# Performance work log

Hardware: AMD Instinct MI355X
Metric: run time of the kernel (lower is better)

The kernel has to match this reference:

```python
import jax, jax.numpy as jnp
import numpy as np
import math

N_LEVELS = 16
F_PER_LEVEL = 2
LOG2_T = 19
T = 1 << LOG2_T
BASE_RES = 16
MAX_RES = 2048
PER_LEVEL_SCALE = (MAX_RES / BASE_RES) ** (1.0 / (N_LEVELS - 1))
BOUND = 0.5
PRIMES = (np.uint32(1), np.uint32(2654435761), np.uint32(805459861))


def _weight_norm(v, g):
    # w = g * v / ||v||_row (torch weight_norm over dim=1)
    return v * (g / jnp.linalg.norm(v, axis=1))[:, None]


def _softplus100(x):
    # torch Softplus(beta=100)
    return jax.nn.softplus(100.0 * x) * 0.01


def hashgrid_encode(x01, table):
    # x01: [N,3] in [0,1]; table: [L, T, F]
    feats = []
    for l in range(N_LEVELS):
        scale = BASE_RES * (PER_LEVEL_SCALE ** l) - 1.0  # tcnn grid scale
        res = int(math.ceil(scale)) + 1
        pos = x01 * scale + 0.5
        pos_floor = jnp.floor(pos)
        w = pos - pos_floor                      # [N,3] trilinear fracs
        c0 = pos_floor.astype(jnp.uint32)        # [N,3] base corner
        dense = (res ** 3) <= T                  # static per level
        acc = jnp.zeros((x01.shape[0], F_PER_LEVEL), dtype=table.dtype)
        for corner in range(8):
            off = [(corner >> d) & 1 for d in range(3)]
            cx = c0[:, 0] + np.uint32(off[0])
            cy = c0[:, 1] + np.uint32(off[1])
            cz = c0[:, 2] + np.uint32(off[2])
            if dense:
                idx = cx + cy * np.uint32(res) + cz * np.uint32(res * res)
            else:
                idx = (cx * PRIMES[0]) ^ (cy * PRIMES[1]) ^ (cz * PRIMES[2])
                idx = idx & np.uint32(T - 1)
            wc = ((w[:, 0] if off[0] else 1.0 - w[:, 0])
                  * (w[:, 1] if off[1] else 1.0 - w[:, 1])
                  * (w[:, 2] if off[2] else 1.0 - w[:, 2]))
            acc = acc + wc[:, None] * table[l, idx.astype(jnp.int32)]
        feats.append(acc)
    return jnp.concatenate(feats, axis=-1)  # [N, 32]


def setup_inputs() -> dict:
    key = jax.random.key(0)
    ks = jax.random.split(key, 4)
    N = 2 ** 21
    x = jax.random.uniform(ks[0], (N, 3), jnp.float32, -BOUND, BOUND)
    table = jax.random.uniform(ks[1], (N_LEVELS, T, F_PER_LEVEL), jnp.float32, -1e-4, 1e-4)
    d_in, d_hid, d_out = 35, 64, 13
    v1 = jax.random.normal(ks[2], (d_hid, d_in), jnp.float32) * (math.sqrt(2) / math.sqrt(d_hid))
    v2 = jax.random.normal(ks[3], (d_out, d_hid), jnp.float32) * 1e-4 + math.sqrt(math.pi) / math.sqrt(d_hid)
    g1 = jnp.linalg.norm(v1, axis=1)
    g2 = jnp.linalg.norm(v2, axis=1)
    b1 = jnp.zeros((d_hid,), jnp.float32)
    b2 = jnp.full((d_out,), -0.5, jnp.float32)  # -sphere_init_radius
    return {"x": x, "table": table, "v1": v1, "g1": g1, "b1": b1,
            "v2": v2, "g2": g2, "b2": b2}


def reference(x, table, v1, g1, b1, v2, g2, b2):
    x01 = jnp.clip((x + BOUND) / (2.0 * BOUND), 0.0, 1.0)
    enc = hashgrid_encode(x01, table)            # [N, 32]
    h = jnp.concatenate([x, enc], axis=1)        # [N, 35]
    w1 = _weight_norm(v1, g1)
    w2 = _weight_norm(v2, g2)
    h = _softplus100(h @ w1.T + b1)
    out = h @ w2.T + b2                          # [N, 13]
    return out
```

## Files before the change

kernel.cpp:

```cpp
#include <hip/hip_runtime.h>
#include <hip/hip_fp16.h>
#include <cstdint>
#include <cmath>

#define NLEV 16
#define NHASH 11
#define NDENSE 5
#define TBL (1u << 19)
#define NBKT 32768

typedef _Float16 half8 __attribute__((ext_vector_type(8)));
typedef float f32x4 __attribute__((ext_vector_type(4)));
typedef float f32x4v __attribute__((ext_vector_type(4)));

struct LevelParams {
    float scale[NLEV];
    uint32_t res[NLEV];
    uint32_t hashed_mask;
};

__device__ __forceinline__ int krow_map(int kr) {
    if (kr <= 2) return kr;
    if (kr >= 4 && kr <= 13) return kr - 1;
    if (kr >= 16 && kr <= 37) return kr - 3;
    return -1;
}

__global__ __launch_bounds__(256) void prep_weights(
    const float* __restrict__ v1, const float* __restrict__ g1,
    const float* __restrict__ v2, const float* __restrict__ g2,
    float* __restrict__ w1t, float* __restrict__ w2n,
    __half* __restrict__ w1f, __half* __restrict__ w2f)
{
    int t = threadIdx.x;
    if (t < 64) {
        float s = 0.f;
        #pragma unroll
        for (int k = 0; k < 35; ++k) { float v = v1[t*35 + k]; s += v*v; }
        float f = g1[t] / sqrtf(s);
        #pragma unroll
        for (int k = 0; k < 35; ++k) w1t[k*64 + t] = v1[t*35 + k] * f;
    } else if (t < 77) {
        int r = t - 64;
        float s = 0.f;
        #pragma unroll
        for (int k = 0; k < 64; ++k) { float v = v2[r*64 + k]; s += v*v; }
        float f = g2[r] / sqrtf(s);
        #pragma unroll
        for (int k = 0; k < 64; ++k) w2n[r*64 + k] = v2[r*64 + k] * f;
    }
    __syncthreads();
    for (int i = t; i < 4096; i += 256) {
        int j = i & 7, lane = (i >> 3) & 63, nt = (i >> 9) & 3, kc = i >> 11;
        int kr = kc*32 + ((lane >> 4) << 3) + j;
        int ncol = nt*16 + (lane & 15);
        int m = krow_map(kr);
        float val = (m >= 0) ? w1t[m*64 + ncol] : 0.f;
        w1f[i] = __float2half(val);
    }
    for (int i = t; i < 1024; i += 256) {
        int j = i & 7, lane = (i >> 3) & 63, kc = i >> 9;
        int kr = kc*32 + ((lane >> 4) << 3) + j;
        int col = lane & 15;
        float val = (col < 13) ? w2n[col*64 + kr] : 0.f;
        w2f[i] = __float2half(val);
    }
}

__global__ __launch_bounds__(256) void pack_table(
    const float2* __restrict__ in, uint32_t* __restrict__ out, int n)
{
    int i = blockIdx.x * 256 + threadIdx.x;
    if (i < n) {
        float2 v = in[i];
        __half2 h = __floats2half2_rn(v.x, v.y);
        out[i] = *reinterpret_cast<uint32_t*>(&h);
    }
}

__device__ __forceinline__ uint32_t bucket_key(float u0, float u1, float u2)
{
    uint32_t a = min(31u, (uint32_t)(u0 * 32.f));
    uint32_t b = min(31u, (uint32_t)(u1 * 32.f));
    uint32_t c = min(31u, (uint32_t)(u2 * 32.f));
    return (a << 10) | (b << 5) | c;
}

__device__ __forceinline__ void load_u(const float* __restrict__ x, int pp,
                                       float& u0, float& u1, float& u2)
{
    float x0 = x[3*(size_t)pp + 0];
    float x1 = x[3*(size_t)pp + 1];
    float x2 = x[3*(size_t)pp + 2];
    u0 = fminf(fmaxf(x0 + 0.5f, 0.f), 1.f);
    u1 = fminf(fmaxf(x1 + 0.5f, 0.f), 1.f);
    u2 = fminf(fmaxf(x2 + 0.5f, 0.f), 1.f);
}

__global__ __launch_bounds__(256) void hist_kernel(
    const float* __restrict__ x, uint32_t* __restrict__ hist, int N)
{
    int i = blockIdx.x * 256 + threadIdx.x;
    if (i < N) {
        float u0, u1, u2;
        load_u(x, i, u0, u1, u2);
        atomicAdd(&hist[bucket_key(u0, u1, u2)], 1u);
    }
}

__global__ __launch_bounds__(1024) void scan_hist(
    const uint32_t* __restrict__ hist, uint32_t* __restrict__ offs)
{
    __shared__ uint32_t part[1024];
    int t = threadIdx.x;
    uint32_t loc[32];
    uint32_t s = 0;
    #pragma unroll
    for (int k = 0; k < 32; ++k) { loc[k] = s; s += hist[t*32 + k]; }
    part[t] = s;
    __syncthreads();
    for (int d = 1; d < 1024; d <<= 1) {
        uint32_t v = (t >= d) ? part[t - d] : 0u;
        __syncthreads();
        part[t] += v;
        __syncthreads();
    }
    uint32_t base = (t > 0) ? part[t - 1] : 0u;
    #pragma unroll
    for (int k = 0; k < 32; ++k) offs[t*32 + k] = base + loc[k];
}

__global__ __launch_bounds__(256) void scatter_kernel(
    const float* __restrict__ x, uint32_t* __restrict__ offs,
    float4* __restrict__ xs4, int N)
{
    int i = blockIdx.x * 256 + threadIdx.x;
    if (i < N) {
        float x0 = x[3*(size_t)i + 0];
        float x1 = x[3*(size_t)i + 1];
        float x2 = x[3*(size_t)i + 2];
        float u0 = fminf(fmaxf(x0 + 0.5f, 0.f), 1.f);
        float u1 = fminf(fmaxf(x1 + 0.5f, 0.f), 1.f);
        float u2 = fminf(fmaxf(x2 + 0.5f, 0.f), 1.f);
        uint32_t pos = atomicAdd(&offs[bucket_key(u0, u1, u2)], 1u);
        xs4[pos] = make_float4(x0, x1, x2, __int_as_float(i));
    }
}

__device__ __forceinline__ void encode_one(
    float u0, float u1, float u2, float s, uint32_t res, bool hashed,
    const uint32_t* __restrict__ tl, float& a0, float& a1)
{
    float px = u0 * s + 0.5f;
    float py = u1 * s + 0.5f;
    float pz = u2 * s + 0.5f;
    float fx = floorf(px), fy = floorf(py), fz = floorf(pz);
    float wx1 = px - fx, wy1 = py - fy, wz1 = pz - fz;
    float wx0 = 1.f - wx1, wy0 = 1.f - wy1, wz0 = 1.f - wz1;
    uint32_t cx = (uint32_t)fx, cy = (uint32_t)fy, cz = (uint32_t)fz;

    uint32_t ix0, ix1, iy0, iy1, iz0, iz1;
    if (hashed) {
        ix0 = cx;                 ix1 = cx + 1u;
        iy0 = cy * 2654435761u;   iy1 = (cy + 1u) * 2654435761u;
        iz0 = cz * 805459861u;    iz1 = (cz + 1u) * 805459861u;
    } else {
        ix0 = cx;                 ix1 = cx + 1u;
        iy0 = cy * res;           iy1 = iy0 + res;
        uint32_t rr = res * res;
        iz0 = cz * rr;            iz1 = iz0 + rr;
    }

    uint32_t idxs[8];
    #pragma unroll
    for (int c = 0; c < 8; ++c) {
        uint32_t jx = (c & 1) ? ix1 : ix0;
        uint32_t jy = (c & 2) ? iy1 : iy0;
        uint32_t jz = (c & 4) ? iz1 : iz0;
        idxs[c] = hashed ? ((jx ^ jy ^ jz) & (TBL - 1u)) : (jx + jy + jz);
    }
    uint32_t raw[8];
    #pragma unroll
    for (int c = 0; c < 8; ++c) raw[c] = tl[idxs[c]];

    float wxy00 = wx0*wy0, wxy10 = wx1*wy0, wxy01 = wx0*wy1, wxy11 = wx1*wy1;
    a0 = 0.f; a1 = 0.f;
    #pragma unroll
    for (int c = 0; c < 8; ++c) {
        float wxy = (c & 2) ? ((c & 1) ? wxy11 : wxy01)
                            : ((c & 1) ? wxy10 : wxy00);
        float w = wxy * ((c & 4) ? wz1 : wz0);
        __half2 hv = *reinterpret_cast<__half2*>(&raw[c]);
        float2 v = __half22float2(hv);
        a0 += w * v.x;
        a1 += w * v.y;
    }
}

template <int SORTED>
__global__ __launch_bounds__(256) void encode_hashed(
    const float* __restrict__ x, const float4* __restrict__ xs4,
    const uint32_t* __restrict__ tpk,
    uint32_t* __restrict__ feats, int N, int chunks_per_level, int lbase,
    LevelParams P)
{
    int bid = blockIdx.x;
    int ll = bid / chunks_per_level;
    int l = lbase + ll;
    int li = l - NDENSE;
    int base = (bid - ll * chunks_per_level) * 512 + threadIdx.x;
    const uint32_t* tl = tpk + (size_t)l * TBL;
    float s = P.scale[l];

    int p[2] = { base, base + 256 };
    uint2 Q[2][4];
    uint32_t par[2];
    float wx0[2], wx1[2], wyz[2][4];

    #pragma unroll
    for (int t = 0; t < 2; ++t) {
        int pp = (p[t] < N) ? p[t] : (N - 1);
        float u0, u1, u2;
        if (SORTED) {
            f32x4v v4 = __builtin_nontemporal_load(
                reinterpret_cast<const f32x4v*>(xs4 + pp));
            u0 = fminf(fmaxf(v4.x + 0.5f, 0.f), 1.f);
            u1 = fminf(fmaxf(v4.y + 0.5f, 0.f), 1.f);
            u2 = fminf(fmaxf(v4.z + 0.5f, 0.f), 1.f);
        } else {
            load_u(x, pp, u0, u1, u2);
        }

        float px = u0 * s + 0.5f;
        float py = u1 * s + 0.5f;
        float pz = u2 * s + 0.5f;
        float fx = floorf(px), fy = floorf(py), fz = floorf(pz);
        float a1f = px - fx, b1f = py - fy, c1f = pz - fz;
        wx1[t] = a1f; wx0[t] = 1.f - a1f;
        float wy0 = 1.f - b1f, wz0 = 1.f - c1f;
        uint32_t cx = (uint32_t)fx, cy = (uint32_t)fy, cz = (uint32_t)fz;

        wyz[t][0] = wy0 * wz0;
        wyz[t][1] = b1f * wz0;
        wyz[t][2] = wy0 * c1f;
        wyz[t][3] = b1f * c1f;

        uint32_t hy0 = cy * 2654435761u, hy1 = (cy + 1u) * 2654435761u;
        uint32_t hz0 = cz * 805459861u,  hz1 = (cz + 1u) * 805459861u;
        uint32_t r[4] = { hy0 ^ hz0, hy1 ^ hz0, hy0 ^ hz1, hy1 ^ hz1 };

        par[t] = 0u;
        if (!(cx & 1u)) {
            #pragma unroll
            for (int k = 0; k < 4; ++k) {
                uint32_t v0 = (cx ^ r[k]) & (TBL - 1u);
                Q[t][k] = *reinterpret_cast<const uint2*>(tl + (v0 & ~1u));
                par[t] |= (v0 & 1u) << k;
            }
        } else {
            #pragma unroll
            for (int k = 0; k < 4; ++k) {
                uint32_t v0 = (cx ^ r[k]) & (TBL - 1u);
                uint32_t v1 = ((cx + 1u) ^ r[k]) & (TBL - 1u);
                Q[t][k].x = tl[v0];
                Q[t][k].y = tl[v1];
            }
        }
    }

    #pragma unroll
    for (int t = 0; t < 2; ++t) {
        float a0 = 0.f, a1 = 0.f;
        #pragma unroll
        for (int k = 0; k < 4; ++k) {
            uint32_t swap = (par[t] >> k) & 1u;
            uint32_t b0 = swap ? Q[t][k].y : Q[t][k].x;
            uint32_t b1 = swap ? Q[t][k].x : Q[t][k].y;
            __half2 h0 = *reinterpret_cast<__half2*>(&b0);
            __half2 h1 = *reinterpret_cast<__half2*>(&b1);
            float2 c0 = __half22float2(h0);
            float2 c1 = __half22float2(h1);
            a0 += wyz[t][k] * (wx0[t] * c0.x + wx1[t] * c1.x);
            a1 += wyz[t][k] * (wx0[t] * c0.y + wx1[t] * c1.y);
        }
        __half2 hv = __floats2half2_rn(a0, a1);
        if (p[t] < N) {
            __builtin_nontemporal_store(*reinterpret_cast<uint32_t*>(&hv),
                                        &feats[(size_t)li * N + p[t]]);
        }
    }
}

__global__ __launch_bounds__(256) void mlp_mfma(
    const float4* __restrict__ xs4,
    const uint32_t* __restrict__ tpk,
    const uint32_t* __restrict__ feats,
    const __half* __restrict__ w1f,
    const __half* __restrict__ w2f,
    const float* __restrict__ b1,
    const float* __restrict__ b2,
    float* __restrict__ out, int N, LevelParams P)
{
    __shared__ uint4 ldsA[4][576];
    __shared__ int   ldsI[4][64];
    int wid = threadIdx.x >> 6, lane = threadIdx.x & 63;
    int wpt = blockIdx.x * 256 + wid * 64;
    int pt = wpt + lane;
    int pp = (pt < N) ? pt : (N - 1);

    f32x4v v4 = __builtin_nontemporal_load(
        reinterpret_cast<const f32x4v*>(xs4 + pp));
    float x0 = v4.x, x1 = v4.y, x2 = v4.z;
    ldsI[wid][lane] = __float_as_int(v4.w);
    float u0 = fminf(fmaxf(x0 + 0.5f, 0.f), 1.f);
    float u1 = fminf(fmaxf(x1 + 0.5f, 0.f), 1.f);
    float u2 = fminf(fmaxf(x2 + 0.5f, 0.f), 1.f);

    uint32_t dw[32];
    #pragma unroll
    for (int i = 0; i < 32; ++i) dw[i] = 0u;
    __half2 h01 = __floats2half2_rn(x0, x1);
    __half2 h2_ = __floats2half2_rn(x2, 0.f);
    dw[0] = *reinterpret_cast<uint32_t*>(&h01);
    dw[1] = *reinterpret_cast<uint32_t*>(&h2_);
    #pragma unroll
    for (int l = 0; l < NDENSE; ++l) {
        const uint32_t* tl = tpk + (size_t)l * TBL;
        float a0, a1;
        encode_one(u0, u1, u2, P.scale[l], P.res[l], false, tl, a0, a1);
        __half2 hv = __floats2half2_rn(a0, a1);
        dw[2 + l] = *reinterpret_cast<uint32_t*>(&hv);
    }
    #pragma unroll
    for (int li = 0; li < NHASH; ++li)
        dw[8 + li] = __builtin_nontemporal_load(&feats[(size_t)li * N + pp]);

    #pragma unroll
    for (int c = 0; c < 8; ++c) {
        uint4 ch = make_uint4(dw[4*c], dw[4*c+1], dw[4*c+2], dw[4*c+3]);
        ldsA[wid][c*64 + lane] = ch;
    }

    const uint4* w1f4 = (const uint4*)w1f;
    half8 bf[4][2];
    #pragma unroll
    for (int nt = 0; nt < 4; ++nt)
        #pragma unroll
        for (int kc = 0; kc < 2; ++kc) {
            uint4 u = w1f4[(kc*4 + nt)*64 + lane];
            bf[nt][kc] = __builtin_bit_cast(half8, u);
        }

    f32x4 C[4][4];
    #pragma unroll
    for (int nt = 0; nt < 4; ++nt) {
        float bv = b1[nt*16 + (lane & 15)];
        #pragma unroll
        for (int m = 0; m < 4; ++m) C[m][nt] = f32x4{bv, bv, bv, bv};
    }

    #pragma unroll
    for (int m = 0; m < 4; ++m) {
        uint4 ua0 = ldsA[wid][((lane >> 4)      )*64 + m*16 + (lane & 15)];
        uint4 ua1 = ldsA[wid][((lane >> 4) + 4  )*64 + m*16 + (lane & 15)];
        half8 a0 = __builtin_bit_cast(half8, ua0);
        half8 a1 = __builtin_bit_cast(half8, ua1);
        #pragma unroll
        for (int nt = 0; nt < 4; ++nt) {
            C[m][nt] = __builtin_amdgcn_mfma_f32_16x16x32_f16(a0, bf[nt][0], C[m][nt], 0, 0, 0);
            C[m][nt] = __builtin_amdgcn_mfma_f32_16x16x32_f16(a1, bf[nt][1], C[m][nt], 0, 0, 0);
        }
    }

    #pragma unroll
    for (int m = 0; m < 4; ++m)
        #pragma unroll
        for (int nt = 0; nt < 4; ++nt)
            #pragma unroll
            for (int r = 0; r < 4; ++r) {
                float z = 100.f * C[m][nt][r];
                float t = __expf(-fabsf(z));
                C[m][nt][r] = (fmaxf(z, 0.f) + __logf(1.f + t)) * 0.01f;
            }

    uint32_t* hl = (uint32_t*)&ldsA[wid][0];
    bool evenl = (lane & 1) == 0;
    #pragma unroll
    for (int m = 0; m < 4; ++m)
        #pragma unroll
        for (int nt = 0; nt < 4; ++nt)
            #pragma unroll
            for (int r = 0; r < 4; ++r) {
                float self = C[m][nt][r];
                float other = __shfl_xor(self, 1);
                if (evenl) {
                    __half2 hp = __floats2half2_rn(self, other);
                    int prow = m*16 + ((lane >> 4) << 2) + r;
                    int colp = (nt*16 + (lane & 15)) >> 1;
                    hl[prow*36 + colp] = *reinterpret_cast<uint32_t*>(&hp);
                }
            }

    const uint4* w2f4 = (const uint4*)w2f;
    half8 b2f[2];
    #pragma unroll
    for (int kc = 0; kc < 2; ++kc) {
        uint4 u = w2f4[kc*64 + lane];
        b2f[kc] = __builtin_bit_cast(half8, u);
    }
    int col = lane & 15;
    float b2v = (col < 13) ? b2[col] : 0.f;

    #pragma unroll
    for (int m = 0; m < 4; ++m) {
        uint4 ua0 = ldsA[wid][(m*16 + col)*9 + 0 + (lane >> 4)];
        uint4 ua1 = ldsA[wid][(m*16 + col)*9 + 4 + (lane >> 4)];
        f32x4 c2 = f32x4{b2v, b2v, b2v, b2v};
        c2 = __builtin_amdgcn_mfma_f32_16x16x32_f16(
                 __builtin_bit_cast(half8, ua0), b2f[0], c2, 0, 0, 0);
        c2 = __builtin_amdgcn_mfma_f32_16x16x32_f16(
                 __builtin_bit_cast(half8, ua1), b2f[1], c2, 0, 0, 0);
        #pragma unroll
        for (int r = 0; r < 4; ++r) {
            int prow = m*16 + ((lane >> 4) << 2) + r;
            if (col < 13 && wpt + prow < N) {
                int og = ldsI[wid][prow];
                out[(size_t)og * 13 + col] = c2[r];
            }
        }
    }
}

__global__ __launch_bounds__(256) void mlp_dense_scalar(
    const float* __restrict__ x, const uint32_t* __restrict__ tpk,
    const uint32_t* __restrict__ feats,
    const float* __restrict__ w1t, const float* __restrict__ b1,
    const float* __restrict__ w2, const float* __restrict__ b2,
    float* __restrict__ out, int N, LevelParams P)
{
    int p = blockIdx.x * 256 + threadIdx.x;
    bool valid = (p < N);
    int pp = valid ? p : (N - 1);

    float x0 = x[3*(size_t)pp + 0];
    float x1 = x[3*(size_t)pp + 1];
    float x2 = x[3*(size_t)pp + 2];
    float u0 = fminf(fmaxf(x0 + 0.5f, 0.f), 1.f);
    float u1 = fminf(fmaxf(x1 + 0.5f, 0.f), 1.f);
    float u2 = fminf(fmaxf(x2 + 0.5f, 0.f), 1.f);

    uint32_t rf[NHASH];
    #pragma unroll
    for (int li = 0; li < NHASH; ++li) rf[li] = feats[(size_t)li * N + pp];

    float h[64];
    #pragma unroll
    for (int j = 0; j < 64; ++j)
        h[j] = b1[j] + x0 * w1t[0*64 + j] + x1 * w1t[1*64 + j] + x2 * w1t[2*64 + j];

    #pragma unroll
    for (int l = 0; l < NDENSE; ++l) {
        const uint32_t* tl = tpk + (size_t)l * TBL;
        float a0, a1;
        encode_one(u0, u1, u2, P.scale[l], P.res[l], false, tl, a0, a1);
        const float* c0p = w1t + (3 + 2*l) * 64;
        const float* c1p = c0p + 64;
        #pragma unroll
        for (int j = 0; j < 64; ++j) h[j] += a0 * c0p[j] + a1 * c1p[j];
    }
    #pragma unroll
    for (int li = 0; li < NHASH; ++li) {
        __half2 hv = *reinterpret_cast<__half2*>(&rf[li]);
        float2 f = __half22float2(hv);
        int l = li + NDENSE;
        const float* c0p = w1t + (3 + 2*l) * 64;
        const float* c1p = c0p + 64;
        #pragma unroll
        for (int j = 0; j < 64; ++j) h[j] += f.x * c0p[j] + f.y * c1p[j];
    }
    #pragma unroll
    for (int j = 0; j < 64; ++j) {
        float z = 100.f * h[j];
        float t = __expf(-fabsf(z));
        h[j] = (fmaxf(z, 0.f) + __logf(1.f + t)) * 0.01f;
    }
    float* op = out + (size_t)pp * 13;
    for (int o = 0; o < 13; ++o) {
        float a = b2[o];
        const float* wr = w2 + o * 64;
        #pragma unroll
        for (int k = 0; k < 64; ++k) a = fmaf(h[k], wr[k], a);
        if (valid) op[o] = a;
    }
}

template <int PACKED>
__global__ __launch_bounds__(256) void sdf_fused(
    const float* __restrict__ x, const void* __restrict__ table,
    const float* __restrict__ w1t, const float* __restrict__ b1,
    const float* __restrict__ w2, const float* __restrict__ b2,
    float* __restrict__ out, int N, LevelParams P)
{
    int i = blockIdx.x * 256 + threadIdx.x;
    bool valid = (i < N);
    int ii = valid ? i : (N - 1);

    float x0 = x[3*(size_t)ii + 0];
    float x1 = x[3*(size_t)ii + 1];
    float x2 = x[3*(size_t)ii + 2];
    float u0 = fminf(fmaxf(x0 + 0.5f, 0.f), 1.f);
    float u1 = fminf(fmaxf(x1 + 0.5f, 0.f), 1.f);
    float u2 = fminf(fmaxf(x2 + 0.5f, 0.f), 1.f);

    float h[64];
    #pragma unroll
    for (int j = 0; j < 64; ++j)
        h[j] = b1[j] + x0 * w1t[0*64 + j] + x1 * w1t[1*64 + j] + x2 * w1t[2*64 + j];

    for (int l = 0; l < NLEV; ++l) {
        bool hashed = (P.hashed_mask >> l) & 1u;
        float a0, a1;
        if (PACKED) {
            const uint32_t* tl = (const uint32_t*)table + (size_t)l * TBL;
            encode_one(u0, u1, u2, P.scale[l], P.res[l], hashed, tl, a0, a1);
        } else {
            const float* tl = (const float*)table + (size_t)l * (size_t)(TBL * 2u);
            float s = P.scale[l]; uint32_t res = P.res[l];
            float px = u0*s + 0.5f, py = u1*s + 0.5f, pz = u2*s + 0.5f;
            float fx = floorf(px), fy = floorf(py), fz = floorf(pz);
            float wx1 = px-fx, wy1 = py-fy, wz1 = pz-fz;
            float wx0 = 1.f-wx1, wy0 = 1.f-wy1, wz0 = 1.f-wz1;
            uint32_t cx = (uint32_t)fx, cy = (uint32_t)fy, cz = (uint32_t)fz;
            a0 = 0.f; a1 = 0.f;
            #pragma unroll
            for (int c = 0; c < 8; ++c) {
                uint32_t jx = cx + (c & 1);
                uint32_t jy = cy + ((c >> 1) & 1);
                uint32_t jz = cz + ((c >> 2) & 1);
                uint32_t idx = hashed
                    ? ((jx ^ (jy * 2654435761u) ^ (jz * 805459861u)) & (TBL - 1u))
                    : (jx + jy * res + jz * res * res);
                float w = ((c & 1) ? wx1 : wx0) * ((c & 2) ? wy1 : wy0)
                        * ((c & 4) ? wz1 : wz0);
                float2 v = *reinterpret_cast<const float2*>(tl + (size_t)idx * 2u);
                a0 += w * v.x; a1 += w * v.y;
            }
        }
        const float* c0p = w1t + (3 + 2*l) * 64;
        const float* c1p = c0p + 64;
        #pragma unroll
        for (int j = 0; j < 64; ++j) h[j] += a0 * c0p[j] + a1 * c1p[j];
    }

    #pragma unroll
    for (int j = 0; j < 64; ++j) {
        float z = 100.f * h[j];
        float t = __expf(-fabsf(z));
        h[j] = (fmaxf(z, 0.f) + __logf(1.f + t)) * 0.01f;
    }

    float* op = out + (size_t)ii * 13;
    for (int o = 0; o < 13; ++o) {
        float a = b2[o];
        const float* wr = w2 + o * 64;
        #pragma unroll
        for (int k = 0; k < 64; ++k) a += h[k] * wr[k];
        if (valid) op[o] = a;
    }
}

extern "C" void kernel_launch(void* const* d_in, const int* in_sizes, int n_in,
                              void* d_out, int out_size, void* d_ws, size_t ws_size,
                              hipStream_t stream)
{
    const float* x     = (const float*)d_in[0];
    const float* table = (const float*)d_in[1];
    const float* v1    = (const float*)d_in[2];
    const float* g1    = (const float*)d_in[3];
    const float* b1    = (const float*)d_in[4];
    const float* v2    = (const float*)d_in[5];
    const float* g2    = (const float*)d_in[6];
    const float* b2    = (const float*)d_in[7];
    float* out = (float*)d_out;
    int N = in_sizes[0] / 3;

    const int n_entries = NLEV * (int)TBL;
    const size_t packed_bytes = (size_t)n_entries * 4u;
    const size_t xs4_bytes    = (size_t)N * 16u;
    const size_t feats_bytes  = (size_t)NHASH * (size_t)N * 4u;
    const size_t hist_bytes   = (size_t)NBKT * 4u;
    const size_t w_bytes      = (35*64 + 13*64) * sizeof(float);
    const size_t wf_bytes     = (4096 + 1024) * sizeof(__half);

    size_t off_packed = 0;
    size_t off_xs4    = off_packed + packed_bytes;
    size_t off_feats  = off_xs4 + xs4_bytes;
    size_t off_hist   = off_feats + feats_bytes;
    size_t off_offs   = off_hist + hist_bytes;
    size_t off_w      = off_offs + hist_bytes;
    size_t off_wf     = off_w + w_bytes;
    size_t sorted_need = off_wf + wf_bytes;

    bool sorted_ok = (ws_size >= sorted_need);
    bool two_pass  = (ws_size >= packed_bytes + feats_bytes + w_bytes + wf_bytes);
    bool packed_ok = (ws_size >= packed_bytes + w_bytes + wf_bytes);

    uint32_t* tpk   = (uint32_t*)((char*)d_ws + off_packed);
    float4*   xs4   = (float4*)((char*)d_ws + off_xs4);
    uint32_t* hist  = (uint32_t*)((char*)d_ws + off_hist);
    uint32_t* offs  = (uint32_t*)((char*)d_ws + off_offs);
    uint32_t* feats;
    float* w1t;
    if (sorted_ok) {
        feats = (uint32_t*)((char*)d_ws + off_feats);
        w1t = (float*)((char*)d_ws + off_w);
    } else if (two_pass) {
        feats = (uint32_t*)((char*)d_ws + packed_bytes);
        w1t = (float*)((char*)d_ws + packed_bytes + feats_bytes);
    } else {
        feats = nullptr;
        w1t = (float*)((char*)d_ws + (packed_ok ? packed_bytes : 0));
    }
    float* w2n = w1t + 35 * 64;
    __half* w1f = (__half*)(w2n + 13 * 64);
    __half* w2f = w1f + 4096;

    LevelParams P;
    P.hashed_mask = 0u;
    double pls = pow(128.0, 1.0 / 15.0);
    for (int l = 0; l < NLEV; ++l) {
        double sc = 16.0 * pow(pls, (double)l) - 1.0;
        P.scale[l] = (float)sc;
        uint32_t res = (uint32_t)(ceil(sc)) + 1u;
        P.res[l] = res;
        uint64_t r3 = (uint64_t)res * res * res;
        if (r3 > (uint64_t)TBL) P.hashed_mask |= (1u << l);
    }

    prep_weights<<<1, 256, 0, stream>>>(v1, g1, v2, g2, w1t, w2n, w1f, w2f);

    int chunks = (N + 255) / 256;
    if (sorted_ok) {
        pack_table<<<(n_entries + 255) / 256, 256, 0, stream>>>(
            (const float2*)table, tpk, n_entries);
        hipMemsetAsync(hist, 0, hist_bytes, stream);
        hist_kernel<<<chunks, 256, 0, stream>>>(x, hist, N);
        scan_hist<<<1, 1024, 0, stream>>>(hist, offs);
        scatter_kernel<<<chunks, 256, 0, stream>>>(x, offs, xs4, N);
        int chunks2 = (N + 511) / 512;
        encode_hashed<1><<<chunks2 * 6, 256, 0, stream>>>(
            x, xs4, tpk, feats, N, chunks2, 5, P);
        encode_hashed<1><<<chunks2 * 5, 256, 0, stream>>>(
            x, xs4, tpk, feats, N, chunks2, 11, P);
        mlp_mfma<<<chunks, 256, 0, stream>>>(
            xs4, tpk, feats, w1f, w2f, b1, b2, out, N, P);
    } else if (two_pass) {
        pack_table<<<(n_entries + 255) / 256, 256, 0, stream>>>(
            (const float2*)table, tpk, n_entries);
        int chunks2 = (N + 511) / 512;
        encode_hashed<0><<<chunks2 * NHASH, 256, 0, stream>>>(
            x, nullptr, tpk, feats, N, chunks2, 5, P);
        mlp_dense_scalar<<<chunks, 256, 0, stream>>>(
            x, tpk, feats, w1t, b1, w2n, b2, out, N, P);
    } else if (packed_ok) {
        pack_table<<<(n_entries + 255) / 256, 256, 0, stream>>>(
            (const float2*)table, tpk, n_entries);
        sdf_fused<1><<<chunks, 256, 0, stream>>>(
            x, (const void*)tpk, w1t, b1, w2n, b2, out, N, P);
    } else {
        sdf_fused<0><<<chunks, 256, 0, stream>>>(
            x, (const void*)table, w1t, b1, w2n, b2, out, N, P);
    }
}
```

Measured before the change: 798.2 us.

## Fuse table pack with histogram; widen hashed gathers to 16-byte aligned loads

```diff
diff --git a/kernel.cpp b/kernel.cpp
--- a/kernel.cpp
+++ b/kernel.cpp
@@ -11,7 +11,6 @@
 
 typedef _Float16 half8 __attribute__((ext_vector_type(8)));
 typedef float f32x4 __attribute__((ext_vector_type(4)));
-typedef float f32x4v __attribute__((ext_vector_type(4)));
 
 struct LevelParams {
     float scale[NLEV];
@@ -67,17 +66,6 @@
     }
 }
 
-__global__ __launch_bounds__(256) void pack_table(
-    const float2* __restrict__ in, uint32_t* __restrict__ out, int n)
-{
-    int i = blockIdx.x * 256 + threadIdx.x;
-    if (i < n) {
-        float2 v = in[i];
-        __half2 h = __floats2half2_rn(v.x, v.y);
-        out[i] = *reinterpret_cast<uint32_t*>(&h);
-    }
-}
-
 __device__ __forceinline__ uint32_t bucket_key(float u0, float u1, float u2)
 {
     uint32_t a = min(31u, (uint32_t)(u0 * 32.f));
@@ -97,14 +85,26 @@
     u2 = fminf(fmaxf(x2 + 0.5f, 0.f), 1.f);
 }
 
-__global__ __launch_bounds__(256) void hist_kernel(
-    const float* __restrict__ x, uint32_t* __restrict__ hist, int N)
-{
-    int i = blockIdx.x * 256 + threadIdx.x;
-    if (i < N) {
-        float u0, u1, u2;
-        load_u(x, i, u0, u1, u2);
-        atomicAdd(&hist[bucket_key(u0, u1, u2)], 1u);
+__global__ __launch_bounds__(256) void pack_and_hist(
+    const float2* __restrict__ tin, uint32_t* __restrict__ tout, int n_entries,
+    const float* __restrict__ x, uint32_t* __restrict__ hist, int N,
+    int packBlocks)
+{
+    int b = blockIdx.x;
+    if (b < packBlocks) {
+        int i = b * 256 + threadIdx.x;
+        if (i < n_entries) {
+            float2 v = tin[i];
+            __half2 h = __floats2half2_rn(v.x, v.y);
+            tout[i] = *reinterpret_cast<uint32_t*>(&h);
+        }
+    } else {
+        int i = (b - packBlocks) * 256 + threadIdx.x;
+        if (i < N) {
+            float u0, u1, u2;
+            load_u(x, i, u0, u1, u2);
+            atomicAdd(&hist[bucket_key(u0, u1, u2)], 1u);
+        }
     }
 }
 
@@ -197,6 +197,13 @@
     }
 }
 
+__device__ __forceinline__ uint32_t sel4(uint4 q, uint32_t p)
+{
+    uint32_t lo = (p & 1u) ? q.y : q.x;
+    uint32_t hi = (p & 1u) ? q.w : q.z;
+    return (p & 2u) ? hi : lo;
+}
+
 template <int SORTED>
 __global__ __launch_bounds__(256) void encode_hashed(
     const float* __restrict__ x, const float4* __restrict__ xs4,
@@ -213,7 +220,7 @@
     float s = P.scale[l];
 
     int p[2] = { base, base + 256 };
-    uint2 Q[2][4];
+    uint4 Q[2][4];
     uint32_t par[2];
     float wx0[2], wx1[2], wyz[2][4];
 
@@ -222,8 +229,7 @@
         int pp = (p[t] < N) ? p[t] : (N - 1);
         float u0, u1, u2;
         if (SORTED) {
-            f32x4v v4 = __builtin_nontemporal_load(
-                reinterpret_cast<const f32x4v*>(xs4 + pp));
+            float4 v4 = xs4[pp];
             u0 = fminf(fmaxf(v4.x + 0.5f, 0.f), 1.f);
             u1 = fminf(fmaxf(v4.y + 0.5f, 0.f), 1.f);
             u2 = fminf(fmaxf(v4.z + 0.5f, 0.f), 1.f);
@@ -249,15 +255,18 @@
         uint32_t hz0 = cz * 805459861u,  hz1 = (cz + 1u) * 805459861u;
         uint32_t r[4] = { hy0 ^ hz0, hy1 ^ hz0, hy0 ^ hz1, hy1 ^ hz1 };
 
-        par[t] = 0u;
-        if (!(cx & 1u)) {
+        if ((cx & 3u) != 3u) {
+            uint32_t pr = 0u;
             #pragma unroll
             for (int k = 0; k < 4; ++k) {
                 uint32_t v0 = (cx ^ r[k]) & (TBL - 1u);
-                Q[t][k] = *reinterpret_cast<const uint2*>(tl + (v0 & ~1u));
-                par[t] |= (v0 & 1u) << k;
+                uint32_t v1 = ((cx + 1u) ^ r[k]) & (TBL - 1u);
+                Q[t][k] = *reinterpret_cast<const uint4*>(tl + (v0 & ~3u));
+                pr |= ((v0 & 3u) << (4*k)) | ((v1 & 3u) << (4*k + 2));
             }
+            par[t] = pr;
         } else {
+            par[t] = 0x80000000u;
             #pragma unroll
             for (int k = 0; k < 4; ++k) {
                 uint32_t v0 = (cx ^ r[k]) & (TBL - 1u);
@@ -270,12 +279,19 @@
 
     #pragma unroll
     for (int t = 0; t < 2; ++t) {
+        bool slow = (par[t] >> 31) != 0u;
         float a0 = 0.f, a1 = 0.f;
         #pragma unroll
         for (int k = 0; k < 4; ++k) {
-            uint32_t swap = (par[t] >> k) & 1u;
-            uint32_t b0 = swap ? Q[t][k].y : Q[t][k].x;
-            uint32_t b1 = swap ? Q[t][k].x : Q[t][k].y;
+            uint32_t b0, b1;
+            if (slow) {
+                b0 = Q[t][k].x;
+                b1 = Q[t][k].y;
+            } else {
+                uint32_t pk = par[t] >> (4*k);
+                b0 = sel4(Q[t][k], pk & 3u);
+                b1 = sel4(Q[t][k], (pk >> 2) & 3u);
+            }
             __half2 h0 = *reinterpret_cast<__half2*>(&b0);
             __half2 h1 = *reinterpret_cast<__half2*>(&b1);
             float2 c0 = __half22float2(h0);
@@ -308,8 +324,7 @@
     int pt = wpt + lane;
     int pp = (pt < N) ? pt : (N - 1);
 
-    f32x4v v4 = __builtin_nontemporal_load(
-        reinterpret_cast<const f32x4v*>(xs4 + pp));
+    float4 v4 = xs4[pp];
     float x0 = v4.x, x1 = v4.y, x2 = v4.z;
     ldsI[wid][lane] = __float_as_int(v4.w);
     float u0 = fminf(fmaxf(x0 + 0.5f, 0.f), 1.f);
@@ -333,7 +348,7 @@
     }
     #pragma unroll
     for (int li = 0; li < NHASH; ++li)
-        dw[8 + li] = __builtin_nontemporal_load(&feats[(size_t)li * N + pp]);
+        dw[8 + li] = feats[(size_t)li * N + pp];
 
     #pragma unroll
     for (int c = 0; c < 8; ++c) {
@@ -640,11 +655,11 @@
     prep_weights<<<1, 256, 0, stream>>>(v1, g1, v2, g2, w1t, w2n, w1f, w2f);
 
     int chunks = (N + 255) / 256;
+    int packBlocks = (n_entries + 255) / 256;
     if (sorted_ok) {
-        pack_table<<<(n_entries + 255) / 256, 256, 0, stream>>>(
-            (const float2*)table, tpk, n_entries);
         hipMemsetAsync(hist, 0, hist_bytes, stream);
-        hist_kernel<<<chunks, 256, 0, stream>>>(x, hist, N);
+        pack_and_hist<<<packBlocks + chunks, 256, 0, stream>>>(
+            (const float2*)table, tpk, n_entries, x, hist, N, packBlocks);
         scan_hist<<<1, 1024, 0, stream>>>(hist, offs);
         scatter_kernel<<<chunks, 256, 0, stream>>>(x, offs, xs4, N);
         int chunks2 = (N + 511) / 512;
@@ -655,16 +670,16 @@
         mlp_mfma<<<chunks, 256, 0, stream>>>(
             xs4, tpk, feats, w1f, w2f, b1, b2, out, N, P);
     } else if (two_pass) {
-        pack_table<<<(n_entries + 255) / 256, 256, 0, stream>>>(
-            (const float2*)table, tpk, n_entries);
+        pack_and_hist<<<packBlocks, 256, 0, stream>>>(
+            (const float2*)table, tpk, n_entries, x, nullptr, 0, packBlocks);
         int chunks2 = (N + 511) / 512;
         encode_hashed<0><<<chunks2 * NHASH, 256, 0, stream>>>(
             x, nullptr, tpk, feats, N, chunks2, 5, P);
         mlp_dense_scalar<<<chunks, 256, 0, stream>>>(
             x, tpk, feats, w1t, b1, w2n, b2, out, N, P);
     } else if (packed_ok) {
-        pack_table<<<(n_entries + 255) / 256, 256, 0, stream>>>(
-            (const float2*)table, tpk, n_entries);
+        pack_and_hist<<<packBlocks, 256, 0, stream>>>(
+            (const float2*)table, tpk, n_entries, x, nullptr, 0, packBlocks);
         sdf_fused<1><<<chunks, 256, 0, stream>>>(
             x, (const void*)tpk, w1t, b1, w2n, b2, out, N, P);
     } else {
```

Result: slower. 924.6 us (+15.8%).
